# Kernel optimization log

Measured on AMD Instinct MI355X. Metric: run time of the kernel, lower is better.

## Reference

```python
import jax, jax.numpy as jnp
import numpy as np

B = 16384
T = 64  # num_taps

def setup_inputs() -> dict:
    key = jax.random.key(0)
    k1, k2 = jax.random.split(key)
    x = jax.random.normal(k1, (B, T), dtype=jnp.float32)
    d = jax.random.normal(k2, (B,), dtype=jnp.float32)
    w_prev = jnp.zeros((B, T), dtype=jnp.float32)
    # standard RLS init: P0 = delta * I, batched
    P_prev = jnp.broadcast_to(jnp.eye(T, dtype=jnp.float32), (B, T, T))
    forgetting_factor = jnp.asarray(0.99, dtype=jnp.float32)
    return {"x": x, "d": d, "w_prev": w_prev, "P_prev": P_prev,
            "forgetting_factor": forgetting_factor}

def reference(x, d, w_prev, P_prev, forgetting_factor):
    lam = jnp.clip(forgetting_factor, 0.0001, 0.9999)
    # Px = P_prev @ x  -> (B, T)
    Px = jnp.einsum('bij,bj->bi', P_prev, x)
    # denom = lambda + x^T P x  -> (B,)
    denom = lam + jnp.einsum('bi,bi->b', x, Px)
    g = Px / denom[:, None]                         # gain (B, T)
    y_hat = jnp.sum(w_prev * x, axis=-1)            # (B,)
    error = d - y_hat
    w_next = w_prev + g * error[:, None]
    # P_update = g (x^T P_prev)  -> rank-1 (B, T, T)
    xP = jnp.einsum('bi,bij->bj', x, P_prev)
    P_next = (P_prev - g[:, :, None] * xP[:, None, :]) / lam
    return (w_next, P_next, y_hat)
```

## Files before the change

### kernel.cpp

```cpp
#include <hip/hip_runtime.h>


constexpr int T = 64;

__global__ __launch_bounds__(256) void rls_step(
    const float* __restrict__ x,
    const float* __restrict__ d,
    const float* __restrict__ w_prev,
    const float* __restrict__ P_prev,
    const float* __restrict__ ffp,
    float* __restrict__ w_next,
    float* __restrict__ P_next,
    float* __restrict__ y_hat)
{
    const int b    = blockIdx.x;
    const int t    = threadIdx.x;
    const int wave = t >> 6;
    const int lane = t & 63;
    const int grp  = t >> 4;
    const int sub  = t & 15;
    const int c0   = sub * 4;

    __shared__ float  x_s[T];
    __shared__ float  w_s[T];
    __shared__ float  Px_s[T];
    __shared__ float4 xPw[4][16];
    __shared__ float  denw[4];

    const float lam     = fminf(fmaxf(ffp[0], 1.0e-4f), 0.9999f);
    const float inv_lam = 1.0f / lam;
    const float db      = d[b];

    const float4* __restrict__ Pv =
        reinterpret_cast<const float4*>(P_prev) + (size_t)b * (T * T / 4);
    float4* __restrict__ Pnv =
        reinterpret_cast<float4*>(P_next) + (size_t)b * (T * T / 4);

    float4 p0 = Pv[0 * 256 + t];
    float4 p1 = Pv[1 * 256 + t];
    float4 p2 = Pv[2 * 256 + t];
    float4 p3 = Pv[3 * 256 + t];

    if (t < 16)
        reinterpret_cast<float4*>(x_s)[t] =
            reinterpret_cast<const float4*>(x + (size_t)b * T)[t];
    else if (t < 32)
        reinterpret_cast<float4*>(w_s)[t - 16] =
            reinterpret_cast<const float4*>(w_prev + (size_t)b * T)[t - 16];
    __syncthreads();

    const float xc0 = x_s[c0 + 0], xc1 = x_s[c0 + 1];
    const float xc2 = x_s[c0 + 2], xc3 = x_s[c0 + 3];
    const float xi0 = x_s[grp +  0];
    const float xi1 = x_s[grp + 16];
    const float xi2 = x_s[grp + 32];
    const float xi3 = x_s[grp + 48];

    float r0 = p0.x * xc0 + p0.y * xc1 + p0.z * xc2 + p0.w * xc3;
    float r1 = p1.x * xc0 + p1.y * xc1 + p1.z * xc2 + p1.w * xc3;
    float r2 = p2.x * xc0 + p2.y * xc1 + p2.z * xc2 + p2.w * xc3;
    float r3 = p3.x * xc0 + p3.y * xc1 + p3.z * xc2 + p3.w * xc3;

    float dpart = xi0 * r0 + xi1 * r1 + xi2 * r2 + xi3 * r3;

    float yp = w_s[lane] * x_s[lane];

    r0 += __shfl_xor(r0, 1); r0 += __shfl_xor(r0, 2); r0 += __shfl_xor(r0, 4); r0 += __shfl_xor(r0, 8);
    r1 += __shfl_xor(r1, 1); r1 += __shfl_xor(r1, 2); r1 += __shfl_xor(r1, 4); r1 += __shfl_xor(r1, 8);
    r2 += __shfl_xor(r2, 1); r2 += __shfl_xor(r2, 2); r2 += __shfl_xor(r2, 4); r2 += __shfl_xor(r2, 8);
    r3 += __shfl_xor(r3, 1); r3 += __shfl_xor(r3, 2); r3 += __shfl_xor(r3, 4); r3 += __shfl_xor(r3, 8);
    if (sub == 0) {
        Px_s[grp +  0] = r0;
        Px_s[grp + 16] = r1;
        Px_s[grp + 32] = r2;
        Px_s[grp + 48] = r3;
    }

    float s0 = xi0 * p0.x + xi1 * p1.x + xi2 * p2.x + xi3 * p3.x;
    float s1 = xi0 * p0.y + xi1 * p1.y + xi2 * p2.y + xi3 * p3.y;
    float s2 = xi0 * p0.z + xi1 * p1.z + xi2 * p2.z + xi3 * p3.z;
    float s3 = xi0 * p0.w + xi1 * p1.w + xi2 * p2.w + xi3 * p3.w;
    s0 += __shfl_xor(s0, 16); s0 += __shfl_xor(s0, 32);
    s1 += __shfl_xor(s1, 16); s1 += __shfl_xor(s1, 32);
    s2 += __shfl_xor(s2, 16); s2 += __shfl_xor(s2, 32);
    s3 += __shfl_xor(s3, 16); s3 += __shfl_xor(s3, 32);
    if (lane < 16) xPw[wave][lane] = make_float4(s0, s1, s2, s3);

    dpart += __shfl_xor(dpart, 1);  dpart += __shfl_xor(dpart, 2);
    dpart += __shfl_xor(dpart, 4);  dpart += __shfl_xor(dpart, 8);
    dpart += __shfl_xor(dpart, 16); dpart += __shfl_xor(dpart, 32);
    if (lane == 0) denw[wave] = dpart;

    yp += __shfl_xor(yp, 1);  yp += __shfl_xor(yp, 2);
    yp += __shfl_xor(yp, 4);  yp += __shfl_xor(yp, 8);
    yp += __shfl_xor(yp, 16); yp += __shfl_xor(yp, 32);
    const float err = db - yp;

    __syncthreads();

    const float inv_den = 1.0f / (lam + denw[0] + denw[1] + denw[2] + denw[3]);

    const float4 q0 = xPw[0][sub], q1 = xPw[1][sub];
    const float4 q2 = xPw[2][sub], q3 = xPw[3][sub];
    const float xq0 = q0.x + q1.x + q2.x + q3.x;
    const float xq1 = q0.y + q1.y + q2.y + q3.y;
    const float xq2 = q0.z + q1.z + q2.z + q3.z;
    const float xq3 = q0.w + q1.w + q2.w + q3.w;

    const float g0 = r0 * inv_den;
    const float g1 = r1 * inv_den;
    const float g2 = r2 * inv_den;
    const float g3 = r3 * inv_den;

    if (t < 64) {
        w_next[(size_t)b * T + t] = w_s[t] + Px_s[t] * inv_den * err;
    } else if (t == 64) {
        y_hat[b] = yp;
    }

    float4 o;
    o.x = (p0.x - g0 * xq0) * inv_lam;
    o.y = (p0.y - g0 * xq1) * inv_lam;
    o.z = (p0.z - g0 * xq2) * inv_lam;
    o.w = (p0.w - g0 * xq3) * inv_lam;
    Pnv[0 * 256 + t] = o;
    o.x = (p1.x - g1 * xq0) * inv_lam;
    o.y = (p1.y - g1 * xq1) * inv_lam;
    o.z = (p1.z - g1 * xq2) * inv_lam;
    o.w = (p1.w - g1 * xq3) * inv_lam;
    Pnv[1 * 256 + t] = o;
    o.x = (p2.x - g2 * xq0) * inv_lam;
    o.y = (p2.y - g2 * xq1) * inv_lam;
    o.z = (p2.z - g2 * xq2) * inv_lam;
    o.w = (p2.w - g2 * xq3) * inv_lam;
    Pnv[2 * 256 + t] = o;
    o.x = (p3.x - g3 * xq0) * inv_lam;
    o.y = (p3.y - g3 * xq1) * inv_lam;
    o.z = (p3.z - g3 * xq2) * inv_lam;
    o.w = (p3.w - g3 * xq3) * inv_lam;
    Pnv[3 * 256 + t] = o;
}

extern "C" void kernel_launch(void* const* d_in, const int* in_sizes, int n_in,
                              void* d_out, int out_size, void* d_ws, size_t ws_size,
                              hipStream_t stream) {
    const float* x      = (const float*)d_in[0];
    const float* d      = (const float*)d_in[1];
    const float* w_prev = (const float*)d_in[2];
    const float* P_prev = (const float*)d_in[3];
    const float* ffp    = (const float*)d_in[4];

    const int B = in_sizes[1];

    float* out    = (float*)d_out;
    float* w_next = out;
    float* P_next = out + (size_t)B * T;
    float* y_hat  = out + (size_t)B * T + (size_t)B * T * T;

    rls_step<<<B, 256, 0, stream>>>(x, d, w_prev, P_prev, ffp,
                                    w_next, P_next, y_hat);
}
```

Baseline: 102.5 us.

## Process each batch matrix in one wave with double-buffered register prefetch

Each 64-lane wave now handles four batch elements in sequence instead of one block per batch element. It keeps two 64-float4 register buffers so the next matrix loads while the current one computes. All reductions use wavefront shuffles, which removes shared memory and __syncthreads. The aim is to hide memory latency and cut per-block overhead on this bandwidth-bound kernel. The cost is much higher register pressure, about 128 VGPRs for the P buffers alone, which lowers occupancy. The grid also shrinks to B/16 blocks.

```diff
diff --git a/kernel.cpp b/kernel.cpp
--- a/kernel.cpp
+++ b/kernel.cpp
@@ -1,7 +1,9 @@
 #include <hip/hip_runtime.h>
 
 
-constexpr int T = 64;
+constexpr int T    = 64;
+constexpr int ROWS = 4;
+constexpr int WPB  = 4;
 
 __global__ __launch_bounds__(256) void rls_step(
     const float* __restrict__ x,
@@ -11,134 +13,109 @@
     const float* __restrict__ ffp,
     float* __restrict__ w_next,
     float* __restrict__ P_next,
-    float* __restrict__ y_hat)
+    float* __restrict__ y_hat,
+    int B)
 {
-    const int b    = blockIdx.x;
-    const int t    = threadIdx.x;
-    const int wave = t >> 6;
-    const int lane = t & 63;
-    const int grp  = t >> 4;
-    const int sub  = t & 15;
-    const int c0   = sub * 4;
+    const int t  = threadIdx.x;
+    const int l  = t & 63;
+    const int gw = blockIdx.x * WPB + (t >> 6);
+    const int b0 = gw * ROWS;
+    if (b0 >= B) return;
 
-    __shared__ float  x_s[T];
-    __shared__ float  w_s[T];
-    __shared__ float  Px_s[T];
-    __shared__ float4 xPw[4][16];
-    __shared__ float  denw[4];
+    const int g   = l >> 4;
+    const int s16 = l & 15;
+    const int c0  = s16 * 4;
 
     const float lam     = fminf(fmaxf(ffp[0], 1.0e-4f), 0.9999f);
     const float inv_lam = 1.0f / lam;
-    const float db      = d[b];
 
-    const float4* __restrict__ Pv =
-        reinterpret_cast<const float4*>(P_prev) + (size_t)b * (T * T / 4);
-    float4* __restrict__ Pnv =
-        reinterpret_cast<float4*>(P_next) + (size_t)b * (T * T / 4);
+    float4 pA[16], pB[16];
+    float  xvA, wvA, dbA;  float4 xcA;
+    float  xvB, wvB, dbB;  float4 xcB;
 
-    float4 p0 = Pv[0 * 256 + t];
-    float4 p1 = Pv[1 * 256 + t];
-    float4 p2 = Pv[2 * 256 + t];
-    float4 p3 = Pv[3 * 256 + t];
+    auto LOADROW = [&](float4 (&p)[16], float& xv, float& wv, float4& xc,
+                       float& db, int bi) {
+        const float4* __restrict__ Pv =
+            reinterpret_cast<const float4*>(P_prev) + (size_t)bi * (T * T / 4);
+        #pragma unroll
+        for (int k = 0; k < 16; ++k) p[k] = Pv[k * 64 + l];
+        xv = x[(size_t)bi * T + l];
+        wv = w_prev[(size_t)bi * T + l];
+        xc = *reinterpret_cast<const float4*>(x + (size_t)bi * T + c0);
+        db = d[bi];
+    };
 
-    if (t < 16)
-        reinterpret_cast<float4*>(x_s)[t] =
-            reinterpret_cast<const float4*>(x + (size_t)b * T)[t];
-    else if (t < 32)
-        reinterpret_cast<float4*>(w_s)[t - 16] =
-            reinterpret_cast<const float4*>(w_prev + (size_t)b * T)[t - 16];
-    __syncthreads();
+    auto DOROW = [&](float4 (&p)[16], float xv, float wv, float4 xc,
+                     float db, int bi) {
+        float xi[16];
+        #pragma unroll
+        for (int k = 0; k < 16; ++k) xi[k] = __shfl(xv, 4 * k + g);
 
-    const float xc0 = x_s[c0 + 0], xc1 = x_s[c0 + 1];
-    const float xc2 = x_s[c0 + 2], xc3 = x_s[c0 + 3];
-    const float xi0 = x_s[grp +  0];
-    const float xi1 = x_s[grp + 16];
-    const float xi2 = x_s[grp + 32];
-    const float xi3 = x_s[grp + 48];
+        float r[16];
+        float dp = 0.0f, s0 = 0.0f, s1 = 0.0f, s2 = 0.0f, s3 = 0.0f;
+        #pragma unroll
+        for (int k = 0; k < 16; ++k) {
+            r[k] = p[k].x * xc.x + p[k].y * xc.y + p[k].z * xc.z + p[k].w * xc.w;
+            dp += xi[k] * r[k];
+            s0 += xi[k] * p[k].x;
+            s1 += xi[k] * p[k].y;
+            s2 += xi[k] * p[k].z;
+            s3 += xi[k] * p[k].w;
+        }
 
-    float r0 = p0.x * xc0 + p0.y * xc1 + p0.z * xc2 + p0.w * xc3;
-    float r1 = p1.x * xc0 + p1.y * xc1 + p1.z * xc2 + p1.w * xc3;
-    float r2 = p2.x * xc0 + p2.y * xc1 + p2.z * xc2 + p2.w * xc3;
-    float r3 = p3.x * xc0 + p3.y * xc1 + p3.z * xc2 + p3.w * xc3;
+        dp += __shfl_xor(dp, 1);  dp += __shfl_xor(dp, 2);  dp += __shfl_xor(dp, 4);
+        dp += __shfl_xor(dp, 8);  dp += __shfl_xor(dp, 16); dp += __shfl_xor(dp, 32);
+        const float inv_den = 1.0f / (lam + dp);
 
-    float dpart = xi0 * r0 + xi1 * r1 + xi2 * r2 + xi3 * r3;
+        s0 += __shfl_xor(s0, 16); s0 += __shfl_xor(s0, 32);
+        s1 += __shfl_xor(s1, 16); s1 += __shfl_xor(s1, 32);
+        s2 += __shfl_xor(s2, 16); s2 += __shfl_xor(s2, 32);
+        s3 += __shfl_xor(s3, 16); s3 += __shfl_xor(s3, 32);
 
-    float yp = w_s[lane] * x_s[lane];
+        float yp = wv * xv;
+        yp += __shfl_xor(yp, 1);  yp += __shfl_xor(yp, 2);  yp += __shfl_xor(yp, 4);
+        yp += __shfl_xor(yp, 8);  yp += __shfl_xor(yp, 16); yp += __shfl_xor(yp, 32);
+        const float err = db - yp;
 
-    r0 += __shfl_xor(r0, 1); r0 += __shfl_xor(r0, 2); r0 += __shfl_xor(r0, 4); r0 += __shfl_xor(r0, 8);
-    r1 += __shfl_xor(r1, 1); r1 += __shfl_xor(r1, 2); r1 += __shfl_xor(r1, 4); r1 += __shfl_xor(r1, 8);
-    r2 += __shfl_xor(r2, 1); r2 += __shfl_xor(r2, 2); r2 += __shfl_xor(r2, 4); r2 += __shfl_xor(r2, 8);
-    r3 += __shfl_xor(r3, 1); r3 += __shfl_xor(r3, 2); r3 += __shfl_xor(r3, 4); r3 += __shfl_xor(r3, 8);
-    if (sub == 0) {
-        Px_s[grp +  0] = r0;
-        Px_s[grp + 16] = r1;
-        Px_s[grp + 32] = r2;
-        Px_s[grp + 48] = r3;
-    }
+        #pragma unroll
+        for (int k = 0; k < 16; ++k) {
+            r[k] += __shfl_xor(r[k], 1); r[k] += __shfl_xor(r[k], 2);
+            r[k] += __shfl_xor(r[k], 4); r[k] += __shfl_xor(r[k], 8);
+        }
 
-    float s0 = xi0 * p0.x + xi1 * p1.x + xi2 * p2.x + xi3 * p3.x;
-    float s1 = xi0 * p0.y + xi1 * p1.y + xi2 * p2.y + xi3 * p3.y;
-    float s2 = xi0 * p0.z + xi1 * p1.z + xi2 * p2.z + xi3 * p3.z;
-    float s3 = xi0 * p0.w + xi1 * p1.w + xi2 * p2.w + xi3 * p3.w;
-    s0 += __shfl_xor(s0, 16); s0 += __shfl_xor(s0, 32);
-    s1 += __shfl_xor(s1, 16); s1 += __shfl_xor(s1, 32);
-    s2 += __shfl_xor(s2, 16); s2 += __shfl_xor(s2, 32);
-    s3 += __shfl_xor(s3, 16); s3 += __shfl_xor(s3, 32);
-    if (lane < 16) xPw[wave][lane] = make_float4(s0, s1, s2, s3);
+        float Pxl = 0.0f;
+        const int srcl = (l & 3) << 4;
+        #pragma unroll
+        for (int k = 0; k < 16; ++k) {
+            const float tk = __shfl(r[k], srcl);
+            if ((l >> 2) == k) Pxl = tk;
+        }
 
-    dpart += __shfl_xor(dpart, 1);  dpart += __shfl_xor(dpart, 2);
-    dpart += __shfl_xor(dpart, 4);  dpart += __shfl_xor(dpart, 8);
-    dpart += __shfl_xor(dpart, 16); dpart += __shfl_xor(dpart, 32);
-    if (lane == 0) denw[wave] = dpart;
+        w_next[(size_t)bi * T + l] = wv + Pxl * inv_den * err;
+        if (l == 0) y_hat[bi] = yp;
 
-    yp += __shfl_xor(yp, 1);  yp += __shfl_xor(yp, 2);
-    yp += __shfl_xor(yp, 4);  yp += __shfl_xor(yp, 8);
-    yp += __shfl_xor(yp, 16); yp += __shfl_xor(yp, 32);
-    const float err = db - yp;
+        float4* __restrict__ Pnv =
+            reinterpret_cast<float4*>(P_next) + (size_t)bi * (T * T / 4);
+        #pragma unroll
+        for (int k = 0; k < 16; ++k) {
+            const float gk = r[k] * inv_den;
+            float4 o;
+            o.x = (p[k].x - gk * s0) * inv_lam;
+            o.y = (p[k].y - gk * s1) * inv_lam;
+            o.z = (p[k].z - gk * s2) * inv_lam;
+            o.w = (p[k].w - gk * s3) * inv_lam;
+            Pnv[k * 64 + l] = o;
+        }
+    };
 
-    __syncthreads();
-
-    const float inv_den = 1.0f / (lam + denw[0] + denw[1] + denw[2] + denw[3]);
-
-    const float4 q0 = xPw[0][sub], q1 = xPw[1][sub];
-    const float4 q2 = xPw[2][sub], q3 = xPw[3][sub];
-    const float xq0 = q0.x + q1.x + q2.x + q3.x;
-    const float xq1 = q0.y + q1.y + q2.y + q3.y;
-    const float xq2 = q0.z + q1.z + q2.z + q3.z;
-    const float xq3 = q0.w + q1.w + q2.w + q3.w;
-
-    const float g0 = r0 * inv_den;
-    const float g1 = r1 * inv_den;
-    const float g2 = r2 * inv_den;
-    const float g3 = r3 * inv_den;
-
-    if (t < 64) {
-        w_next[(size_t)b * T + t] = w_s[t] + Px_s[t] * inv_den * err;
-    } else if (t == 64) {
-        y_hat[b] = yp;
-    }
-
-    float4 o;
-    o.x = (p0.x - g0 * xq0) * inv_lam;
-    o.y = (p0.y - g0 * xq1) * inv_lam;
-    o.z = (p0.z - g0 * xq2) * inv_lam;
-    o.w = (p0.w - g0 * xq3) * inv_lam;
-    Pnv[0 * 256 + t] = o;
-    o.x = (p1.x - g1 * xq0) * inv_lam;
-    o.y = (p1.y - g1 * xq1) * inv_lam;
-    o.z = (p1.z - g1 * xq2) * inv_lam;
-    o.w = (p1.w - g1 * xq3) * inv_lam;
-    Pnv[1 * 256 + t] = o;
-    o.x = (p2.x - g2 * xq0) * inv_lam;
-    o.y = (p2.y - g2 * xq1) * inv_lam;
-    o.z = (p2.z - g2 * xq2) * inv_lam;
-    o.w = (p2.w - g2 * xq3) * inv_lam;
-    Pnv[2 * 256 + t] = o;
-    o.x = (p3.x - g3 * xq0) * inv_lam;
-    o.y = (p3.y - g3 * xq1) * inv_lam;
-    o.z = (p3.z - g3 * xq2) * inv_lam;
-    o.w = (p3.w - g3 * xq3) * inv_lam;
-    Pnv[3 * 256 + t] = o;
+    LOADROW(pA, xvA, wvA, xcA, dbA, b0 + 0);
+    LOADROW(pB, xvB, wvB, xcB, dbB, b0 + 1);
+    DOROW  (pA, xvA, wvA, xcA, dbA, b0 + 0);
+    LOADROW(pA, xvA, wvA, xcA, dbA, b0 + 2);
+    DOROW  (pB, xvB, wvB, xcB, dbB, b0 + 1);
+    LOADROW(pB, xvB, wvB, xcB, dbB, b0 + 3);
+    DOROW  (pA, xvA, wvA, xcA, dbA, b0 + 2);
+    DOROW  (pB, xvB, wvB, xcB, dbB, b0 + 3);
 }
 
 extern "C" void kernel_launch(void* const* d_in, const int* in_sizes, int n_in,
@@ -157,6 +134,9 @@
     float* P_next = out + (size_t)B * T;
     float* y_hat  = out + (size_t)B * T + (size_t)B * T * T;
 
-    rls_step<<<B, 256, 0, stream>>>(x, d, w_prev, P_prev, ffp,
-                                    w_next, P_next, y_hat);
+    const int rows_per_block = WPB * ROWS;
+    const int grid = (B + rows_per_block - 1) / rows_per_block;
+
+    rls_step<<<grid, 256, 0, stream>>>(x, d, w_prev, P_prev, ffp,
+                                       w_next, P_next, y_hat, B);
 }
```

Result: slower. 113.8 us (+11.0%).

## Remove first barrier by reading x/w into registers and broadcasting via shuffles

Applied to the files above, without the earlier changes.

Each thread now loads x and w_prev straight from global memory and gets the row-x values with wave shuffles, so the shared-memory staging and the first __syncthreads are gone. The P tile mapping changes so each wave owns a contiguous 16-row slab, which keeps the shuffle broadcast inside one wave. Launch bounds now ask for 8 blocks per CU. The cost is redundant global loads of x per thread (mostly cache hits) and possibly more register pressure from the occupancy hint.

```diff
diff --git a/kernel.cpp b/kernel.cpp
--- a/kernel.cpp
+++ b/kernel.cpp
@@ -3,7 +3,7 @@
 
 constexpr int T = 64;
 
-__global__ __launch_bounds__(256) void rls_step(
+__global__ __launch_bounds__(256, 8) void rls_step(
     const float* __restrict__ x,
     const float* __restrict__ d,
     const float* __restrict__ w_prev,
@@ -13,19 +13,16 @@
     float* __restrict__ P_next,
     float* __restrict__ y_hat)
 {
-    const int b    = blockIdx.x;
-    const int t    = threadIdx.x;
-    const int wave = t >> 6;
-    const int lane = t & 63;
-    const int grp  = t >> 4;
-    const int sub  = t & 15;
-    const int c0   = sub * 4;
+    const int b = blockIdx.x;
+    const int t = threadIdx.x;
+    const int w = t >> 6;
+    const int l = t & 63;
+    const int s16 = l & 15;
+    const int c0  = s16 * 4;
 
-    __shared__ float  x_s[T];
-    __shared__ float  w_s[T];
-    __shared__ float  Px_s[T];
     __shared__ float4 xPw[4][16];
     __shared__ float  denw[4];
+    __shared__ float  Px_s[T];
 
     const float lam     = fminf(fmaxf(ffp[0], 1.0e-4f), 0.9999f);
     const float inv_lam = 1.0f / lam;
@@ -36,45 +33,30 @@
     float4* __restrict__ Pnv =
         reinterpret_cast<float4*>(P_next) + (size_t)b * (T * T / 4);
 
-    float4 p0 = Pv[0 * 256 + t];
-    float4 p1 = Pv[1 * 256 + t];
-    float4 p2 = Pv[2 * 256 + t];
-    float4 p3 = Pv[3 * 256 + t];
+    float4 p0 = Pv[256 * w +   0 + l];
+    float4 p1 = Pv[256 * w +  64 + l];
+    float4 p2 = Pv[256 * w + 128 + l];
+    float4 p3 = Pv[256 * w + 192 + l];
 
-    if (t < 16)
-        reinterpret_cast<float4*>(x_s)[t] =
-            reinterpret_cast<const float4*>(x + (size_t)b * T)[t];
-    else if (t < 32)
-        reinterpret_cast<float4*>(w_s)[t - 16] =
-            reinterpret_cast<const float4*>(w_prev + (size_t)b * T)[t - 16];
-    __syncthreads();
+    const float  xv = x[(size_t)b * T + l];
+    const float  wv = w_prev[(size_t)b * T + l];
+    const float4 xc = *reinterpret_cast<const float4*>(x + (size_t)b * T + c0);
 
-    const float xc0 = x_s[c0 + 0], xc1 = x_s[c0 + 1];
-    const float xc2 = x_s[c0 + 2], xc3 = x_s[c0 + 3];
-    const float xi0 = x_s[grp +  0];
-    const float xi1 = x_s[grp + 16];
-    const float xi2 = x_s[grp + 32];
-    const float xi3 = x_s[grp + 48];
+    const int rbase = 16 * w + (l >> 4);
+    const float xi0 = __shfl(xv, rbase + 0);
+    const float xi1 = __shfl(xv, rbase + 4);
+    const float xi2 = __shfl(xv, rbase + 8);
+    const float xi3 = __shfl(xv, rbase + 12);
 
-    float r0 = p0.x * xc0 + p0.y * xc1 + p0.z * xc2 + p0.w * xc3;
-    float r1 = p1.x * xc0 + p1.y * xc1 + p1.z * xc2 + p1.w * xc3;
-    float r2 = p2.x * xc0 + p2.y * xc1 + p2.z * xc2 + p2.w * xc3;
-    float r3 = p3.x * xc0 + p3.y * xc1 + p3.z * xc2 + p3.w * xc3;
+    float r0 = p0.x * xc.x + p0.y * xc.y + p0.z * xc.z + p0.w * xc.w;
+    float r1 = p1.x * xc.x + p1.y * xc.y + p1.z * xc.z + p1.w * xc.w;
+    float r2 = p2.x * xc.x + p2.y * xc.y + p2.z * xc.z + p2.w * xc.w;
+    float r3 = p3.x * xc.x + p3.y * xc.y + p3.z * xc.z + p3.w * xc.w;
 
-    float dpart = xi0 * r0 + xi1 * r1 + xi2 * r2 + xi3 * r3;
-
-    float yp = w_s[lane] * x_s[lane];
-
-    r0 += __shfl_xor(r0, 1); r0 += __shfl_xor(r0, 2); r0 += __shfl_xor(r0, 4); r0 += __shfl_xor(r0, 8);
-    r1 += __shfl_xor(r1, 1); r1 += __shfl_xor(r1, 2); r1 += __shfl_xor(r1, 4); r1 += __shfl_xor(r1, 8);
-    r2 += __shfl_xor(r2, 1); r2 += __shfl_xor(r2, 2); r2 += __shfl_xor(r2, 4); r2 += __shfl_xor(r2, 8);
-    r3 += __shfl_xor(r3, 1); r3 += __shfl_xor(r3, 2); r3 += __shfl_xor(r3, 4); r3 += __shfl_xor(r3, 8);
-    if (sub == 0) {
-        Px_s[grp +  0] = r0;
-        Px_s[grp + 16] = r1;
-        Px_s[grp + 32] = r2;
-        Px_s[grp + 48] = r3;
-    }
+    float dp = xi0 * r0 + xi1 * r1 + xi2 * r2 + xi3 * r3;
+    dp += __shfl_xor(dp, 1);  dp += __shfl_xor(dp, 2);  dp += __shfl_xor(dp, 4);
+    dp += __shfl_xor(dp, 8);  dp += __shfl_xor(dp, 16); dp += __shfl_xor(dp, 32);
+    if (l == 0) denw[w] = dp;
 
     float s0 = xi0 * p0.x + xi1 * p1.x + xi2 * p2.x + xi3 * p3.x;
     float s1 = xi0 * p0.y + xi1 * p1.y + xi2 * p2.y + xi3 * p3.y;
@@ -84,61 +66,65 @@
     s1 += __shfl_xor(s1, 16); s1 += __shfl_xor(s1, 32);
     s2 += __shfl_xor(s2, 16); s2 += __shfl_xor(s2, 32);
     s3 += __shfl_xor(s3, 16); s3 += __shfl_xor(s3, 32);
-    if (lane < 16) xPw[wave][lane] = make_float4(s0, s1, s2, s3);
+    if (l < 16) xPw[w][l] = make_float4(s0, s1, s2, s3);
 
-    dpart += __shfl_xor(dpart, 1);  dpart += __shfl_xor(dpart, 2);
-    dpart += __shfl_xor(dpart, 4);  dpart += __shfl_xor(dpart, 8);
-    dpart += __shfl_xor(dpart, 16); dpart += __shfl_xor(dpart, 32);
-    if (lane == 0) denw[wave] = dpart;
+    float yp = wv * xv;
+    yp += __shfl_xor(yp, 1);  yp += __shfl_xor(yp, 2);  yp += __shfl_xor(yp, 4);
+    yp += __shfl_xor(yp, 8);  yp += __shfl_xor(yp, 16); yp += __shfl_xor(yp, 32);
+    const float err = db - yp;
 
-    yp += __shfl_xor(yp, 1);  yp += __shfl_xor(yp, 2);
-    yp += __shfl_xor(yp, 4);  yp += __shfl_xor(yp, 8);
-    yp += __shfl_xor(yp, 16); yp += __shfl_xor(yp, 32);
-    const float err = db - yp;
+    r0 += __shfl_xor(r0, 1); r0 += __shfl_xor(r0, 2); r0 += __shfl_xor(r0, 4); r0 += __shfl_xor(r0, 8);
+    r1 += __shfl_xor(r1, 1); r1 += __shfl_xor(r1, 2); r1 += __shfl_xor(r1, 4); r1 += __shfl_xor(r1, 8);
+    r2 += __shfl_xor(r2, 1); r2 += __shfl_xor(r2, 2); r2 += __shfl_xor(r2, 4); r2 += __shfl_xor(r2, 8);
+    r3 += __shfl_xor(r3, 1); r3 += __shfl_xor(r3, 2); r3 += __shfl_xor(r3, 4); r3 += __shfl_xor(r3, 8);
+    if (s16 == 0) {
+        Px_s[rbase + 0]  = r0;
+        Px_s[rbase + 4]  = r1;
+        Px_s[rbase + 8]  = r2;
+        Px_s[rbase + 12] = r3;
+    }
 
     __syncthreads();
 
     const float inv_den = 1.0f / (lam + denw[0] + denw[1] + denw[2] + denw[3]);
 
-    const float4 q0 = xPw[0][sub], q1 = xPw[1][sub];
-    const float4 q2 = xPw[2][sub], q3 = xPw[3][sub];
+    const float4 q0 = xPw[0][s16], q1 = xPw[1][s16];
+    const float4 q2 = xPw[2][s16], q3 = xPw[3][s16];
     const float xq0 = q0.x + q1.x + q2.x + q3.x;
     const float xq1 = q0.y + q1.y + q2.y + q3.y;
     const float xq2 = q0.z + q1.z + q2.z + q3.z;
     const float xq3 = q0.w + q1.w + q2.w + q3.w;
 
+    if (w == 0) {
+        w_next[(size_t)b * T + l] = wv + Px_s[l] * inv_den * err;
+        if (l == 0) y_hat[b] = yp;
+    }
+
     const float g0 = r0 * inv_den;
     const float g1 = r1 * inv_den;
     const float g2 = r2 * inv_den;
     const float g3 = r3 * inv_den;
-
-    if (t < 64) {
-        w_next[(size_t)b * T + t] = w_s[t] + Px_s[t] * inv_den * err;
-    } else if (t == 64) {
-        y_hat[b] = yp;
-    }
-
     float4 o;
     o.x = (p0.x - g0 * xq0) * inv_lam;
     o.y = (p0.y - g0 * xq1) * inv_lam;
     o.z = (p0.z - g0 * xq2) * inv_lam;
     o.w = (p0.w - g0 * xq3) * inv_lam;
-    Pnv[0 * 256 + t] = o;
+    Pnv[256 * w +   0 + l] = o;
     o.x = (p1.x - g1 * xq0) * inv_lam;
     o.y = (p1.y - g1 * xq1) * inv_lam;
     o.z = (p1.z - g1 * xq2) * inv_lam;
     o.w = (p1.w - g1 * xq3) * inv_lam;
-    Pnv[1 * 256 + t] = o;
+    Pnv[256 * w +  64 + l] = o;
     o.x = (p2.x - g2 * xq0) * inv_lam;
     o.y = (p2.y - g2 * xq1) * inv_lam;
     o.z = (p2.z - g2 * xq2) * inv_lam;
     o.w = (p2.w - g2 * xq3) * inv_lam;
-    Pnv[2 * 256 + t] = o;
+    Pnv[256 * w + 128 + l] = o;
     o.x = (p3.x - g3 * xq0) * inv_lam;
     o.y = (p3.y - g3 * xq1) * inv_lam;
     o.z = (p3.z - g3 * xq2) * inv_lam;
     o.w = (p3.w - g3 * xq3) * inv_lam;
-    Pnv[3 * 256 + t] = o;
+    Pnv[256 * w + 192 + l] = o;
 }
 
 extern "C" void kernel_launch(void* const* d_in, const int* in_sizes, int n_in,
```

After: 100.6 us. Within noise of the previous version (-1.9%).
